# Kernel optimization log

Hardware: AMD Instinct MI355X
Metric: run time of the kernel (lower is better)

Reference implementation:

```python
import jax, jax.numpy as jnp
import numpy as np

PC_RANGE = (-59.9, -59.9, -2.0, 59.9, 59.9, 5.9)
TEMPERATURE = 0.1
LOSS_SCALE = 0.01


def setup_inputs() -> dict:
    key = jax.random.key(0)
    k1, k2, k3, k4, k5 = jax.random.split(key, 5)
    B, C, H, W = 4, 128, 512, 512
    N, Ns, Nd = 500, 250, 250
    sf = jax.random.normal(k1, (B, C, H, W), dtype=jnp.float32)
    # x,y inside point-cloud range so pixel indices are valid
    xy = jax.random.uniform(k2, (B, N, 2), minval=-59.0, maxval=59.0)
    rest = jax.random.uniform(k3, (B, N, 5))  # z,h,w,l,yaw (unused by loss)
    flags = jnp.tile(
        jnp.concatenate([jnp.zeros((Ns, 1)), jnp.ones((Nd, 1))], axis=0)[None],
        (B, 1, 1),
    )
    gt_boxes = jnp.concatenate([xy, rest, flags], axis=-1).astype(jnp.float32)
    # reified torch.randint labels: static rows point at a random dynamic row and vice versa
    static_labels = (Ns + jax.random.randint(k4, (Ns,), 0, Nd)).astype(jnp.int32)
    dynamic_labels = jax.random.randint(k5, (Nd,), 0, Ns).astype(jnp.int32)
    return {
        "spatial_features_2d": sf,
        "gt_boxes": gt_boxes,
        "static_labels": static_labels,
        "dynamic_labels": dynamic_labels,
        "num_static": Ns,
    }


def reference(spatial_features_2d, gt_boxes, static_labels, dynamic_labels, num_static):
    B, C, H, W = spatial_features_2d.shape
    # Source bug preserved: only the last batch element's lists survive the loop.
    boxes = gt_boxes[B - 1]  # [N, 8]
    x, y = boxes[:, 0], boxes[:, 1]
    span_w = PC_RANGE[3] - PC_RANGE[0]
    span_h = PC_RANGE[4] - PC_RANGE[1]
    cx = jnp.clip(((x - PC_RANGE[0]) / span_w * W).astype(jnp.int32), 0, W - 1)
    cy = jnp.clip(((y - PC_RANGE[1]) / span_h * H).astype(jnp.int32), 0, H - 1)
    # Vectorized per-box pixel gather: [C, N] -> [N, C]
    feats = spatial_features_2d[B - 1][:, cy, cx].T
    # F.normalize(bev_map, dim=0, p=2) at the gathered pixel (eps=1e-12)
    feats = feats / jnp.maximum(
        jnp.linalg.norm(feats, axis=-1, keepdims=True), 1e-12
    )
    # boxes are laid out static-first, so cat([static, dynamic]) == feats
    # nn.CosineSimilarity (eps=1e-8) then / temperature
    f = feats / jnp.maximum(jnp.linalg.norm(feats, axis=-1, keepdims=True), 1e-8)
    sim = (f @ f.T) / TEMPERATURE  # [N, N]
    labels = jnp.concatenate([static_labels, dynamic_labels], axis=0)
    logp = jax.nn.log_softmax(sim, axis=-1)
    loss = -jnp.mean(jnp.take_along_axis(logp, labels[:, None], axis=1))
    return loss * LOSS_SCALE
```

## Files before the change

### kernel.cpp

```cpp
#include <hip/hip_runtime.h>

constexpr int B = 4, C = 128, H = 512, W = 512, N = 500;
constexpr float PC0   = -59.9f;
constexpr float SPAN  = 119.8f;
constexpr float INV_TEMP = 10.0f;
constexpr float LOSS_SCALE = 0.01f;

__global__ void gather_norm_kernel(const float* __restrict__ sf,
                                   const float* __restrict__ gt,
                                   float* __restrict__ f) {
    const int i = blockIdx.x;
    const int c = threadIdx.x;

    const float x = gt[((size_t)(B - 1) * N + i) * 8 + 0];
    const float y = gt[((size_t)(B - 1) * N + i) * 8 + 1];

    int cx = (int)((x - PC0) / SPAN * (float)W);
    cx = min(max(cx, 0), W - 1);
    int cy = (int)((y - PC0) / SPAN * (float)H);
    cy = min(max(cy, 0), H - 1);

    const float v = sf[(size_t)(B - 1) * C * H * W +
                       (size_t)c * H * W + (size_t)cy * W + (size_t)cx];

    __shared__ float red[128];
    red[c] = v * v;
    __syncthreads();
    for (int s = 64; s > 0; s >>= 1) {
        if (c < s) red[c] += red[c + s];
        __syncthreads();
    }
    const float n1 = fmaxf(sqrtf(red[0]), 1e-12f);
    __syncthreads();

    const float v1 = v / n1;
    red[c] = v1 * v1;
    __syncthreads();
    for (int s = 64; s > 0; s >>= 1) {
        if (c < s) red[c] += red[c + s];
        __syncthreads();
    }
    const float n2 = fmaxf(sqrtf(red[0]), 1e-8f);

    f[(size_t)i * 128 + c] = v1 / n2;
}

__global__ void row_loss_kernel(const float* __restrict__ f,
                                const int* __restrict__ slab,
                                const int* __restrict__ dlab,
                                const int* __restrict__ ns_ptr,
                                float* __restrict__ row_loss) {
    const int i = blockIdx.x;
    const int t = threadIdx.x;
    const int Ns = ns_ptr[0];

    __shared__ float fi[128];
    if (t < 128) fi[t] = f[(size_t)i * 128 + t];
    __shared__ float sh_slabel;
    __syncthreads();

    const int label = (i < Ns) ? slab[i] : dlab[i - Ns];

    const float4* fi4 = (const float4*)fi;
    float sv[2];
    const int jv[2] = { t, t + 256 };

    #pragma unroll
    for (int k = 0; k < 2; ++k) {
        const int j = jv[k];
        if (j < N) {
            const float4* fj = (const float4*)(f + (size_t)j * 128);
            float acc = 0.f;
            #pragma unroll
            for (int c = 0; c < 32; ++c) {
                const float4 a = fi4[c];
                const float4 b = fj[c];
                acc += a.x * b.x + a.y * b.y + a.z * b.z + a.w * b.w;
            }
            acc *= INV_TEMP;
            if (j == label) sh_slabel = acc;
            sv[k] = acc;
        } else {
            sv[k] = -1e30f;
        }
    }

    __shared__ float red[256];
    red[t] = fmaxf(sv[0], sv[1]);
    __syncthreads();
    for (int s = 128; s > 0; s >>= 1) {
        if (t < s) red[t] = fmaxf(red[t], red[t + s]);
        __syncthreads();
    }
    const float mx = red[0];
    __syncthreads();

    float e = 0.f;
    if (jv[0] < N) e += expf(sv[0] - mx);
    if (jv[1] < N) e += expf(sv[1] - mx);
    red[t] = e;
    __syncthreads();
    for (int s = 128; s > 0; s >>= 1) {
        if (t < s) red[t] += red[t + s];
        __syncthreads();
    }

    if (t == 0) {
        const float lse = mx + logf(red[0]);
        row_loss[i] = lse - sh_slabel;
    }
}

__global__ void final_reduce_kernel(const float* __restrict__ row_loss,
                                    float* __restrict__ out) {
    const int t = threadIdx.x;
    float a = 0.f;
    for (int j = t; j < N; j += 256) a += row_loss[j];
    __shared__ float red[256];
    red[t] = a;
    __syncthreads();
    for (int s = 128; s > 0; s >>= 1) {
        if (t < s) red[t] += red[t + s];
        __syncthreads();
    }
    if (t == 0) out[0] = red[0] * (LOSS_SCALE / (float)N);
}

extern "C" void kernel_launch(void* const* d_in, const int* in_sizes, int n_in,
                              void* d_out, int out_size, void* d_ws, size_t ws_size,
                              hipStream_t stream) {
    const float* sf   = (const float*)d_in[0];
    const float* gt   = (const float*)d_in[1];
    const int*   slab = (const int*)d_in[2];
    const int*   dlab = (const int*)d_in[3];
    const int*   nsp  = (const int*)d_in[4];

    float* f        = (float*)d_ws;
    float* row_loss = f + (size_t)N * 128;

    gather_norm_kernel<<<N, 128, 0, stream>>>(sf, gt, f);
    row_loss_kernel<<<N, 256, 0, stream>>>(f, slab, dlab, nsp, row_loss);
    final_reduce_kernel<<<1, 256, 0, stream>>>(row_loss, (float*)d_out);
}
```

Measured before the change: 588.5 us.

## Replace shared-memory tree reductions with wavefront shuffle reductions

Replaces the log-step shared-memory reductions, each step ending in a barrier, with 64-lane xor-shuffle reductions in all three kernels. The gather kernel is also remapped so that one wavefront handles one box, with each lane loading two channels. Four boxes share a 256-thread block and the output is written as float2. The aim is to cut barrier and LDS traffic in these small, latency-bound kernels. The runtime is likely dominated by launch overhead and scattered global reads, so the benefit may be small.

```diff
diff --git a/kernel.cpp b/kernel.cpp
--- a/kernel.cpp
+++ b/kernel.cpp
@@ -6,11 +6,24 @@
 constexpr float INV_TEMP = 10.0f;
 constexpr float LOSS_SCALE = 0.01f;
 
-__global__ void gather_norm_kernel(const float* __restrict__ sf,
-                                   const float* __restrict__ gt,
-                                   float* __restrict__ f) {
-    const int i = blockIdx.x;
-    const int c = threadIdx.x;
+__device__ __forceinline__ float wave_reduce_sum(float v) {
+    #pragma unroll
+    for (int m = 1; m < 64; m <<= 1) v += __shfl_xor(v, m, 64);
+    return v;
+}
+__device__ __forceinline__ float wave_reduce_max(float v) {
+    #pragma unroll
+    for (int m = 1; m < 64; m <<= 1) v = fmaxf(v, __shfl_xor(v, m, 64));
+    return v;
+}
+
+__global__ __launch_bounds__(256) void gather_norm_kernel(
+        const float* __restrict__ sf,
+        const float* __restrict__ gt,
+        float* __restrict__ f) {
+    const int wave = threadIdx.x >> 6;
+    const int lane = threadIdx.x & 63;
+    const int i = blockIdx.x * 4 + wave;
 
     const float x = gt[((size_t)(B - 1) * N + i) * 8 + 0];
     const float y = gt[((size_t)(B - 1) * N + i) * 8 + 1];
@@ -20,54 +33,45 @@
     int cy = (int)((y - PC0) / SPAN * (float)H);
     cy = min(max(cy, 0), H - 1);
 
-    const float v = sf[(size_t)(B - 1) * C * H * W +
-                       (size_t)c * H * W + (size_t)cy * W + (size_t)cx];
+    const float* base = sf + (size_t)(B - 1) * C * H * W + (size_t)cy * W + cx;
+    float v0 = base[(size_t)(2 * lane)     * (H * W)];
+    float v1 = base[(size_t)(2 * lane + 1) * (H * W)];
 
-    __shared__ float red[128];
-    red[c] = v * v;
-    __syncthreads();
-    for (int s = 64; s > 0; s >>= 1) {
-        if (c < s) red[c] += red[c + s];
-        __syncthreads();
-    }
-    const float n1 = fmaxf(sqrtf(red[0]), 1e-12f);
-    __syncthreads();
+    const float s1 = wave_reduce_sum(v0 * v0 + v1 * v1);
+    const float n1 = fmaxf(sqrtf(s1), 1e-12f);
+    v0 /= n1; v1 /= n1;
 
-    const float v1 = v / n1;
-    red[c] = v1 * v1;
-    __syncthreads();
-    for (int s = 64; s > 0; s >>= 1) {
-        if (c < s) red[c] += red[c + s];
-        __syncthreads();
-    }
-    const float n2 = fmaxf(sqrtf(red[0]), 1e-8f);
+    const float s2 = wave_reduce_sum(v0 * v0 + v1 * v1);
+    const float n2 = fmaxf(sqrtf(s2), 1e-8f);
 
-    f[(size_t)i * 128 + c] = v1 / n2;
+    float2 o = make_float2(v0 / n2, v1 / n2);
+    *(float2*)(f + (size_t)i * 128 + 2 * lane) = o;
 }
 
-__global__ void row_loss_kernel(const float* __restrict__ f,
-                                const int* __restrict__ slab,
-                                const int* __restrict__ dlab,
-                                const int* __restrict__ ns_ptr,
-                                float* __restrict__ row_loss) {
+__global__ __launch_bounds__(256) void row_loss_kernel(
+        const float* __restrict__ f,
+        const int* __restrict__ slab,
+        const int* __restrict__ dlab,
+        const int* __restrict__ ns_ptr,
+        float* __restrict__ row_loss) {
     const int i = blockIdx.x;
     const int t = threadIdx.x;
+    const int wave = t >> 6, lane = t & 63;
     const int Ns = ns_ptr[0];
 
     __shared__ float fi[128];
+    __shared__ float sh_slabel;
+    __shared__ float wred[4];
     if (t < 128) fi[t] = f[(size_t)i * 128 + t];
-    __shared__ float sh_slabel;
     __syncthreads();
 
     const int label = (i < Ns) ? slab[i] : dlab[i - Ns];
+    const float4* fi4 = (const float4*)fi;
 
-    const float4* fi4 = (const float4*)fi;
     float sv[2];
-    const int jv[2] = { t, t + 256 };
-
     #pragma unroll
     for (int k = 0; k < 2; ++k) {
-        const int j = jv[k];
+        const int j = t + 256 * k;
         if (j < N) {
             const float4* fj = (const float4*)(f + (size_t)j * 128);
             float acc = 0.f;
@@ -85,45 +89,41 @@
         }
     }
 
-    __shared__ float red[256];
-    red[t] = fmaxf(sv[0], sv[1]);
+    float wm = wave_reduce_max(fmaxf(sv[0], sv[1]));
+    if (lane == 0) wred[wave] = wm;
     __syncthreads();
-    for (int s = 128; s > 0; s >>= 1) {
-        if (t < s) red[t] = fmaxf(red[t], red[t + s]);
-        __syncthreads();
-    }
-    const float mx = red[0];
+    const float mx = fmaxf(fmaxf(wred[0], wred[1]), fmaxf(wred[2], wred[3]));
+
+    float e = 0.f;
+    if (t < N)       e += expf(sv[0] - mx);
+    if (t + 256 < N) e += expf(sv[1] - mx);
+    float ws = wave_reduce_sum(e);
+    __syncthreads();
+    if (lane == 0) wred[wave] = ws;
     __syncthreads();
 
-    float e = 0.f;
-    if (jv[0] < N) e += expf(sv[0] - mx);
-    if (jv[1] < N) e += expf(sv[1] - mx);
-    red[t] = e;
-    __syncthreads();
-    for (int s = 128; s > 0; s >>= 1) {
-        if (t < s) red[t] += red[t + s];
-        __syncthreads();
-    }
-
     if (t == 0) {
-        const float lse = mx + logf(red[0]);
+        const float tot = (wred[0] + wred[1]) + (wred[2] + wred[3]);
+        const float lse = mx + logf(tot);
         row_loss[i] = lse - sh_slabel;
     }
 }
 
-__global__ void final_reduce_kernel(const float* __restrict__ row_loss,
-                                    float* __restrict__ out) {
+__global__ __launch_bounds__(256) void final_reduce_kernel(
+        const float* __restrict__ row_loss,
+        float* __restrict__ out) {
     const int t = threadIdx.x;
+    const int lane = t & 63, wave = t >> 6;
     float a = 0.f;
     for (int j = t; j < N; j += 256) a += row_loss[j];
-    __shared__ float red[256];
-    red[t] = a;
+    float ws = wave_reduce_sum(a);
+    __shared__ float wred[4];
+    if (lane == 0) wred[wave] = ws;
     __syncthreads();
-    for (int s = 128; s > 0; s >>= 1) {
-        if (t < s) red[t] += red[t + s];
-        __syncthreads();
+    if (t == 0) {
+        const float tot = (wred[0] + wred[1]) + (wred[2] + wred[3]);
+        out[0] = tot * (LOSS_SCALE / (float)N);
     }
-    if (t == 0) out[0] = red[0] * (LOSS_SCALE / (float)N);
 }
 
 extern "C" void kernel_launch(void* const* d_in, const int* in_sizes, int n_in,
@@ -138,7 +138,7 @@
     float* f        = (float*)d_ws;
     float* row_loss = f + (size_t)N * 128;
 
-    gather_norm_kernel<<<N, 128, 0, stream>>>(sf, gt, f);
+    gather_norm_kernel<<<125, 256, 0, stream>>>(sf, gt, f);
     row_loss_kernel<<<N, 256, 0, stream>>>(f, slab, dlab, nsp, row_loss);
     final_reduce_kernel<<<1, 256, 0, stream>>>(row_loss, (float*)d_out);
 }
```

Result: no change. 582.9 us (-1.0%).
